# Performance work log

Measured on AMD Instinct MI355X. Metric: run time of the kernel, lower is better.

Reference implementation:

```python
import jax, jax.numpy as jnp
import numpy as np

N_NODES = 20000
N_EDGES = 256000
F_IN = 1024
HID = 1000
N_CLS = 1000
NEG_SLOPE = 0.2


def _glorot(key, shape):
    fan_in, fan_out = shape[1], shape[0]
    lim = np.sqrt(6.0 / (fan_in + fan_out))
    return jax.random.uniform(key, shape, jnp.float32, -lim, lim)


def setup_inputs() -> dict:
    key = jax.random.key(0)
    ks = jax.random.split(key, 16)
    x = jax.random.normal(ks[0], (N_NODES, F_IN), jnp.float32)
    edge_index = jax.random.randint(ks[1], (2, N_EDGES), 0, N_NODES, jnp.int64)
    edge_attr = jax.random.uniform(ks[2], (N_EDGES, 1), jnp.float32)
    return {
        "x": x,
        "edge_index": edge_index,
        "edge_attr": edge_attr,
        # conv1 params (GATv2Conv: F_IN -> HID, heads=1, edge_dim=1)
        "w1_l": _glorot(ks[3], (HID, F_IN)),
        "b1_l": jnp.zeros((HID,), jnp.float32),
        "w1_r": _glorot(ks[4], (HID, F_IN)),
        "b1_r": jnp.zeros((HID,), jnp.float32),
        "w1_e": _glorot(ks[5], (HID, 1)),
        "att1": _glorot(ks[6], (1, HID))[0],
        "bias1": jnp.zeros((HID,), jnp.float32),
        # conv2 params (HID -> N_CLS, heads=1, concat=False)
        "w2_l": _glorot(ks[7], (N_CLS, HID)),
        "b2_l": jnp.zeros((N_CLS,), jnp.float32),
        "w2_r": _glorot(ks[8], (N_CLS, HID)),
        "b2_r": jnp.zeros((N_CLS,), jnp.float32),
        "w2_e": _glorot(ks[9], (N_CLS, 1)),
        "att2": _glorot(ks[10], (1, N_CLS))[0],
        "bias2": jnp.zeros((N_CLS,), jnp.float32),
    }


def gatv2_layer(x, src, dst, edge_attr, Wl, bl, Wr, br, We, att, bias):
    # GATv2Conv with heads=1 (eval mode: attention dropout inactive).
    n = x.shape[0]
    xl = x @ Wl.T + bl                       # source-side transform [N, C]
    xr = x @ Wr.T + br                       # target-side transform [N, C]
    e = xl[src] + xr[dst] + edge_attr @ We.T  # per-edge features [E, C]
    e = jax.nn.leaky_relu(e, NEG_SLOPE)
    logits = e @ att                          # [E]
    # segment softmax over incoming edges of each target node
    m = jax.ops.segment_max(logits, dst, num_segments=n)
    alpha = jnp.exp(logits - m[dst])
    denom = jax.ops.segment_sum(alpha, dst, num_segments=n)
    alpha = alpha / (denom[dst] + 1e-16)
    out = jax.ops.segment_sum(xl[src] * alpha[:, None], dst, num_segments=n)
    return out + bias


def reference(x, edge_index, edge_attr,
              w1_l, b1_l, w1_r, b1_r, w1_e, att1, bias1,
              w2_l, b2_l, w2_r, b2_r, w2_e, att2, bias2):
    src, dst = edge_index[0], edge_index[1]
    # feature dropout (p=0.6) is identity in eval mode
    h = gatv2_layer(x, src, dst, edge_attr, w1_l, b1_l, w1_r, b1_r, w1_e, att1, bias1)
    h = jax.nn.relu(h)
    h = gatv2_layer(h, src, dst, edge_attr, w2_l, b2_l, w2_r, b2_r, w2_e, att2, bias2)
    return jax.nn.sigmoid(h)
```

## Files before the change

### kernel.cpp

```cpp
#include <hip/hip_runtime.h>
#include <math.h>

#define N_NODES 20000
#define N_EDGES 256000
#define F_IN 1024
#define C_DIM 1000
#define NEG_SLOPE 0.2f

#define MPAD 20096
#define KDIM 1024
#define NW 2048

typedef __attribute__((ext_vector_type(8))) short          bf16x8;
typedef __attribute__((ext_vector_type(8))) unsigned short u16x8;
typedef __attribute__((ext_vector_type(4))) float          f32x4;
typedef unsigned short us;

__device__ __forceinline__ us f2bf(float f) {
  unsigned u = __float_as_uint(f);
  return (us)((u + 0x7FFFu + ((u >> 16) & 1u)) >> 16);
}
__device__ __forceinline__ float bf2f(us u) {
  return __uint_as_float(((unsigned)u) << 16);
}

__device__ __forceinline__ void gld16(void* lds, const void* g) {
  __builtin_amdgcn_global_load_lds(
      (const __attribute__((address_space(1))) unsigned int*)g,
      (__attribute__((address_space(3))) unsigned int*)lds, 16, 0, 0);
}

__global__ void count_k(const int* __restrict__ edst, int* __restrict__ counts) {
  int e = blockIdx.x * blockDim.x + threadIdx.x;
  if (e < N_EDGES) atomicAdd(&counts[edst[e]], 1);
}

__global__ __launch_bounds__(1024)
void scan_k(const int* __restrict__ counts, int* __restrict__ row_ptr, int* __restrict__ cursor) {
  __shared__ int sm[1024];
  int t = threadIdx.x;
  int base = t * 20;
  int loc[20];
  int run = 0;
#pragma unroll
  for (int i = 0; i < 20; ++i) {
    int idx = base + i;
    int v = (idx < N_NODES) ? counts[idx] : 0;
    run += v;
    loc[i] = run;
  }
  sm[t] = run;
  __syncthreads();
  for (int off = 1; off < 1024; off <<= 1) {
    int v = (t >= off) ? sm[t - off] : 0;
    __syncthreads();
    sm[t] += v;
    __syncthreads();
  }
  int excl = (t > 0) ? sm[t - 1] : 0;
#pragma unroll
  for (int i = 0; i < 20; ++i) {
    int idx = base + i;
    if (idx < N_NODES) {
      int e = excl + ((i > 0) ? loc[i - 1] : 0);
      row_ptr[idx] = e;
      cursor[idx] = e;
    }
  }
  if (t == 0) row_ptr[N_NODES] = sm[1023];
}

__global__ void scatter_k(const int* __restrict__ esrc, const float* __restrict__ eattr,
                          const int* __restrict__ edst, int* __restrict__ cursor,
                          int2* __restrict__ spair) {
  int e = blockIdx.x * blockDim.x + threadIdx.x;
  if (e < N_EDGES) {
    int p = atomicAdd(&cursor[edst[e]], 1);
    spair[p] = make_int2(esrc[e], __float_as_int(eattr[e]));
  }
}

__global__ void cvt_pad_k(const float* __restrict__ src, us* __restrict__ dst,
                          int R, int C, int dstRows) {
  long total = (long)dstRows * 256;
  for (long i = (long)blockIdx.x * blockDim.x + threadIdx.x; i < total;
       i += (long)gridDim.x * blockDim.x) {
    int row = (int)(i >> 8);
    int c = ((int)(i & 255)) << 2;
    ushort4 o = make_ushort4(0, 0, 0, 0);
    if (row < R && c < C) {
      float4 v = *(const float4*)(src + (long)row * C + c);
      o.x = f2bf(v.x); o.y = f2bf(v.y); o.z = f2bf(v.z); o.w = f2bf(v.w);
    }
    *(ushort4*)(dst + ((long)row << 10) + c) = o;
  }
}

__global__ __launch_bounds__(256)
void gemm_mfma_k(const us* __restrict__ Abf, const us* __restrict__ Wbf,
                 const float* __restrict__ bl, const float* __restrict__ br,
                 us* __restrict__ Cbf) {
  __shared__ us As0[4096], As1[4096], Bs0[4096], Bs1[4096];
  const int tid = threadIdx.x;
  const int lane = tid & 63;
  const int wv = tid >> 6;
  const int wr = wv >> 1, wc = wv & 1;

  const int nwg = gridDim.x;
  const int q = nwg >> 3;
  const int wg = (blockIdx.x & 7) * q + (blockIdx.x >> 3);
  const long bm = (long)(wg >> 4) * 128;
  const long bn = (long)(wg & 15) * 128;

  f32x4 acc[4][4];
  const f32x4 z4 = {0.f, 0.f, 0.f, 0.f};
#pragma unroll
  for (int i = 0; i < 4; ++i)
#pragma unroll
    for (int j = 0; j < 4; ++j) acc[i][j] = z4;

  const int i0 = tid, i1 = tid + 256;
  const us* gA0 = Abf + (bm + (i0 >> 2)) * KDIM + (i0 & 3) * 8;
  const us* gA1 = Abf + (bm + (i1 >> 2)) * KDIM + (i1 & 3) * 8;
  const us* gB0 = Wbf + (bn + (i0 >> 2)) * KDIM + (i0 & 3) * 8;
  const us* gB1 = Wbf + (bn + (i1 >> 2)) * KDIM + (i1 & 3) * 8;

  const int g = lane >> 4;
  const int rA = lane & 15;

  gld16(As0 + wv * 512, gA0);
  gld16(As0 + 2048 + wv * 512, gA1);
  gld16(Bs0 + wv * 512, gB0);
  gld16(Bs0 + 2048 + wv * 512, gB1);
  __syncthreads();

  for (int t = 0; t < 32; ++t) {
    if (t + 1 < 32) {
      int kn = (t + 1) << 5;
      us* dA = ((t + 1) & 1) ? As1 : As0;
      us* dB = ((t + 1) & 1) ? Bs1 : Bs0;
      gld16(dA + wv * 512, gA0 + kn);
      gld16(dA + 2048 + wv * 512, gA1 + kn);
      gld16(dB + wv * 512, gB0 + kn);
      gld16(dB + 2048 + wv * 512, gB1 + kn);
    }
    const us* Ar = (t & 1) ? As1 : As0;
    const us* Br = (t & 1) ? Bs1 : Bs0;
    bf16x8 av[4], bv[4];
#pragma unroll
    for (int mi = 0; mi < 4; ++mi)
      av[mi] = *(const bf16x8*)&Ar[(wr * 64 + mi * 16 + rA) * 32 + g * 8];
#pragma unroll
    for (int ni = 0; ni < 4; ++ni)
      bv[ni] = *(const bf16x8*)&Br[(wc * 64 + ni * 16 + rA) * 32 + g * 8];
#pragma unroll
    for (int mi = 0; mi < 4; ++mi)
#pragma unroll
      for (int ni = 0; ni < 4; ++ni)
        acc[mi][ni] = __builtin_amdgcn_mfma_f32_16x16x32_bf16(av[mi], bv[ni], acc[mi][ni], 0, 0, 0);
    __syncthreads();
  }

  int coln[4]; float biasv[4]; int cok[4];
#pragma unroll
  for (int ni = 0; ni < 4; ++ni) {
    coln[ni] = (int)bn + wc * 64 + ni * 16 + rA;
    int cm = coln[ni] & 1023;
    cok[ni] = (cm < C_DIM);
    biasv[ni] = cok[ni] ? ((coln[ni] < 1024) ? bl[cm] : br[cm]) : 0.f;
  }
#pragma unroll
  for (int mi = 0; mi < 4; ++mi) {
#pragma unroll
    for (int j = 0; j < 4; ++j) {
      int row = (int)bm + wr * 64 + mi * 16 + g * 4 + j;
      if (row < N_NODES) {
#pragma unroll
        for (int ni = 0; ni < 4; ++ni)
          if (cok[ni])
            Cbf[(long)row * NW + coln[ni]] = f2bf(acc[mi][ni][j] + biasv[ni]);
      }
    }
  }
}

template <int ACT>
__global__ __launch_bounds__(256)
void edge_agg_k(const us* __restrict__ xlr, const int2* __restrict__ spair,
                const int* __restrict__ row_ptr,
                const float* __restrict__ We, const float* __restrict__ att,
                const float* __restrict__ bias, us* __restrict__ hout,
                float* __restrict__ fout) {
  const int wave = threadIdx.x >> 6;
  const int lane = threadIdx.x & 63;
  const int q0 = lane, q1 = lane + 64;
  const bool ok1 = (q1 < 125);

  const int d = (blockIdx.x << 2) | wave;
  if (d >= N_NODES) return;

  float attv[2][8], wev[2][8];
#pragma unroll
  for (int j = 0; j < 2; ++j) {
    int qq = lane + 64 * j;
    if (qq < 125) {
      float4 a0 = ((const float4*)att)[2 * qq], a1 = ((const float4*)att)[2 * qq + 1];
      float4 w0 = ((const float4*)We)[2 * qq],  w1 = ((const float4*)We)[2 * qq + 1];
      attv[j][0] = a0.x; attv[j][1] = a0.y; attv[j][2] = a0.z; attv[j][3] = a0.w;
      attv[j][4] = a1.x; attv[j][5] = a1.y; attv[j][6] = a1.z; attv[j][7] = a1.w;
      wev[j][0] = w0.x; wev[j][1] = w0.y; wev[j][2] = w0.z; wev[j][3] = w0.w;
      wev[j][4] = w1.x; wev[j][5] = w1.y; wev[j][6] = w1.z; wev[j][7] = w1.w;
    } else {
#pragma unroll
      for (int t = 0; t < 8; ++t) { attv[j][t] = 0.f; wev[j][t] = 0.f; }
    }
  }

  const int beg = row_ptr[d];
  const int end = row_ptr[d + 1];

  float xrv[2][8];
  {
    const u16x8* xrp = (const u16x8*)(xlr + (long)d * NW + 1024);
#pragma unroll
    for (int j = 0; j < 2; ++j) {
      int qq = lane + 64 * j;
      if (qq < 125) {
        u16x8 h = xrp[qq];
#pragma unroll
        for (int t = 0; t < 8; ++t) xrv[j][t] = bf2f(h[t]);
      } else {
#pragma unroll
        for (int t = 0; t < 8; ++t) xrv[j][t] = 0.f;
      }
    }
  }

  float m = -INFINITY, denom = 0.f;
  float acc[2][8];
#pragma unroll
  for (int j = 0; j < 2; ++j)
#pragma unroll
    for (int t = 0; t < 8; ++t) acc[j][t] = 0.f;

#define EDGE_LOGIT(PAIR, VH0, VH1, PART)                                   \
  {                                                                        \
    const u16x8* xs = (const u16x8*)(xlr + (long)(PAIR).x * NW);           \
    float ea = __int_as_float((PAIR).y);                                   \
    VH0 = xs[q0];                                                          \
    if (ok1) VH1 = xs[q1];                                                 \
    else { u16x8 zz = {0,0,0,0,0,0,0,0}; VH1 = zz; }                       \
    PART = 0.f;                                                            \
    _Pragma("unroll")                                                      \
    for (int t = 0; t < 8; ++t) {                                          \
      float tt = bf2f(VH0[t]) + xrv[0][t] + ea * wev[0][t];                \
      tt = (tt >= 0.f) ? tt : NEG_SLOPE * tt;                              \
      PART = fmaf(attv[0][t], tt, PART);                                   \
      float uu = bf2f(VH1[t]) + xrv[1][t] + ea * wev[1][t];                \
      uu = (uu >= 0.f) ? uu : NEG_SLOPE * uu;                              \
      PART = fmaf(attv[1][t], uu, PART);                                   \
    }                                                                      \
  }

#define ONLINE_UPDATE(PART, VH0, VH1)                                      \
  {                                                                        \
    if ((PART) > m) {                                                      \
      float sc = __expf(m - (PART));                                       \
      denom = denom * sc + 1.f;                                            \
      _Pragma("unroll")                                                    \
      for (int t = 0; t < 8; ++t) {                                        \
        acc[0][t] = fmaf(acc[0][t], sc, bf2f(VH0[t]));                     \
        acc[1][t] = fmaf(acc[1][t], sc, bf2f(VH1[t]));                     \
      }                                                                    \
      m = (PART);                                                          \
    } else {                                                               \
      float w = __expf((PART) - m);                                        \
      denom += w;                                                          \
      _Pragma("unroll")                                                    \
      for (int t = 0; t < 8; ++t) {                                        \
        acc[0][t] = fmaf(w, bf2f(VH0[t]), acc[0][t]);                      \
        acc[1][t] = fmaf(w, bf2f(VH1[t]), acc[1][t]);                      \
      }                                                                    \
    }                                                                      \
  }

  int i = beg;
  for (; i + 2 <= end; i += 2) {
    int2 p0 = spair[i], p1 = spair[i + 1];
    u16x8 a0, a1, b0, b1;
    float pt0, pt1;
    EDGE_LOGIT(p0, a0, a1, pt0);
    EDGE_LOGIT(p1, b0, b1, pt1);
#pragma unroll
    for (int off = 32; off > 0; off >>= 1) {
      pt0 += __shfl_xor(pt0, off, 64);
      pt1 += __shfl_xor(pt1, off, 64);
    }
    ONLINE_UPDATE(pt0, a0, a1);
    ONLINE_UPDATE(pt1, b0, b1);
  }
  if (i < end) {
    int2 p0 = spair[i];
    u16x8 a0, a1;
    float pt0;
    EDGE_LOGIT(p0, a0, a1, pt0);
#pragma unroll
    for (int off = 32; off > 0; off >>= 1) pt0 += __shfl_xor(pt0, off, 64);
    ONLINE_UPDATE(pt0, a0, a1);
  }
#undef EDGE_LOGIT
#undef ONLINE_UPDATE

  float inv = 1.f / (denom + 1e-16f);
  if (ACT == 0) {
    us* orow = hout + ((long)d << 10);
#pragma unroll
    for (int j = 0; j < 2; ++j) {
      int qq = lane + 64 * j;
      u16x8 pk = {0, 0, 0, 0, 0, 0, 0, 0};
      if (qq < 125) {
        const float4 b0 = ((const float4*)bias)[2 * qq], b1 = ((const float4*)bias)[2 * qq + 1];
        const float bb[8] = {b0.x, b0.y, b0.z, b0.w, b1.x, b1.y, b1.z, b1.w};
#pragma unroll
        for (int t = 0; t < 8; ++t)
          pk[t] = f2bf(fmaxf(fmaf(acc[j][t], inv, bb[t]), 0.f));
      }
      ((u16x8*)orow)[qq] = pk;
    }
  } else {
#pragma unroll
    for (int j = 0; j < 2; ++j) {
      int qq = lane + 64 * j;
      if (qq < 125) {
        const float4 b0 = ((const float4*)bias)[2 * qq], b1 = ((const float4*)bias)[2 * qq + 1];
        const float bb[8] = {b0.x, b0.y, b0.z, b0.w, b1.x, b1.y, b1.z, b1.w};
        float o[8];
#pragma unroll
        for (int t = 0; t < 8; ++t)
          o[t] = 1.f / (1.f + __expf(-fmaf(acc[j][t], inv, bb[t])));
        float4* op = (float4*)(fout + (long)d * C_DIM + 8 * qq);
        op[0] = make_float4(o[0], o[1], o[2], o[3]);
        op[1] = make_float4(o[4], o[5], o[6], o[7]);
      }
    }
  }
}

extern "C" void kernel_launch(void* const* d_in, const int* in_sizes, int n_in,
                              void* d_out, int out_size, void* d_ws, size_t ws_size,
                              hipStream_t stream) {
  const float* x     = (const float*)d_in[0];
  const int*   ei    = (const int*)d_in[1];
  const float* eattr = (const float*)d_in[2];
  const float* w1l   = (const float*)d_in[3];
  const float* b1l   = (const float*)d_in[4];
  const float* w1r   = (const float*)d_in[5];
  const float* b1r   = (const float*)d_in[6];
  const float* w1e   = (const float*)d_in[7];
  const float* att1  = (const float*)d_in[8];
  const float* bias1 = (const float*)d_in[9];
  const float* w2l   = (const float*)d_in[10];
  const float* b2l   = (const float*)d_in[11];
  const float* w2r   = (const float*)d_in[12];
  const float* b2r   = (const float*)d_in[13];
  const float* w2e   = (const float*)d_in[14];
  const float* att2  = (const float*)d_in[15];
  const float* bias2 = (const float*)d_in[16];
  float* out = (float*)d_out;

  char* w = (char*)d_ws;
  us*  xlr  = (us*)w;
  us*  Abf  = (us*)(w + 82313216L);
  us*  W21  = (us*)(w + 123469824L);
  us*  W22  = (us*)(w + 127664128L);
  int2* spair = (int2*)(w + 131858432L);
  int* row_ptr = (int*)(w + 133906432L);
  int* cursor  = row_ptr + (N_NODES + 1);
  int* counts  = cursor + N_NODES;

  const int* esrc = ei;
  const int* edst = ei + N_EDGES;

  hipMemsetAsync(counts, 0, N_NODES * sizeof(int), stream);
  count_k<<<(N_EDGES + 255) / 256, 256, 0, stream>>>(edst, counts);
  scan_k<<<1, 1024, 0, stream>>>(counts, row_ptr, cursor);
  scatter_k<<<(N_EDGES + 255) / 256, 256, 0, stream>>>(esrc, eattr, edst, cursor, spair);

  cvt_pad_k<<<1024, 256, 0, stream>>>(w1l, W21, C_DIM, F_IN, 1024);
  cvt_pad_k<<<1024, 256, 0, stream>>>(w1r, W21 + 1024 * 1024, C_DIM, F_IN, 1024);
  cvt_pad_k<<<1024, 256, 0, stream>>>(w2l, W22, C_DIM, C_DIM, 1024);
  cvt_pad_k<<<1024, 256, 0, stream>>>(w2r, W22 + 1024 * 1024, C_DIM, C_DIM, 1024);

  cvt_pad_k<<<4096, 256, 0, stream>>>(x, Abf, N_NODES, F_IN, MPAD);
  gemm_mfma_k<<<2512, 256, 0, stream>>>(Abf, W21, b1l, b1r, xlr);
  edge_agg_k<0><<<N_NODES / 4, 256, 0, stream>>>(xlr, spair, row_ptr, w1e, att1, bias1,
                                                 Abf, nullptr);

  gemm_mfma_k<<<2512, 256, 0, stream>>>(Abf, W22, b2l, b2r, xlr);
  edge_agg_k<1><<<N_NODES / 4, 256, 0, stream>>>(xlr, spair, row_ptr, w2e, att2, bias2,
                                                 nullptr, out);
}
```

Measured before the change: 524.9 us.

## Enlarge GEMM tiles to 256x256 with triple-buffered LDS pipeline and swizzle

The bf16 MFMA GEMM moves from 128x128 tiles with 256 threads and double buffering to 256x256 tiles with 512 threads (8 waves, each computing 128x64). It uses a 3-stage global-to-LDS prefetch ring with explicit vmcnt waits and an XOR swizzle on LDS rows to reduce bank conflicts. The MFMA block is wrapped in setprio. M padding grows to a multiple of 256 and the workspace offsets move to match. The aim is more operand reuse per LDS load and better overlap of loads with math. In exchange the kernel needs much more LDS (about 96KB per block), which limits occupancy, and there are fewer workgroups to spread across the CUs.

```diff
diff --git a/kernel.cpp b/kernel.cpp
--- a/kernel.cpp
+++ b/kernel.cpp
@@ -7,7 +7,7 @@
 #define C_DIM 1000
 #define NEG_SLOPE 0.2f
 
-#define MPAD 20096
+#define MPAD 20224
 #define KDIM 1024
 #define NW 2048
 
@@ -96,70 +96,97 @@
   }
 }
 
-__global__ __launch_bounds__(256)
+__global__ __launch_bounds__(512, 2)
 void gemm_mfma_k(const us* __restrict__ Abf, const us* __restrict__ Wbf,
                  const float* __restrict__ bl, const float* __restrict__ br,
                  us* __restrict__ Cbf) {
-  __shared__ us As0[4096], As1[4096], Bs0[4096], Bs1[4096];
+  __shared__ us As[3 * 8192];
+  __shared__ us Bs[3 * 8192];
   const int tid = threadIdx.x;
   const int lane = tid & 63;
   const int wv = tid >> 6;
-  const int wr = wv >> 1, wc = wv & 1;
-
-  const int nwg = gridDim.x;
-  const int q = nwg >> 3;
-  const int wg = (blockIdx.x & 7) * q + (blockIdx.x >> 3);
-  const long bm = (long)(wg >> 4) * 128;
-  const long bn = (long)(wg & 15) * 128;
-
-  f32x4 acc[4][4];
-  const f32x4 z4 = {0.f, 0.f, 0.f, 0.f};
-#pragma unroll
-  for (int i = 0; i < 4; ++i)
-#pragma unroll
-    for (int j = 0; j < 4; ++j) acc[i][j] = z4;
-
-  const int i0 = tid, i1 = tid + 256;
-  const us* gA0 = Abf + (bm + (i0 >> 2)) * KDIM + (i0 & 3) * 8;
-  const us* gA1 = Abf + (bm + (i1 >> 2)) * KDIM + (i1 & 3) * 8;
-  const us* gB0 = Wbf + (bn + (i0 >> 2)) * KDIM + (i0 & 3) * 8;
-  const us* gB1 = Wbf + (bn + (i1 >> 2)) * KDIM + (i1 & 3) * 8;
-
+  const int wr = wv >> 2;
+  const int wc = wv & 3;
   const int g = lane >> 4;
   const int rA = lane & 15;
 
-  gld16(As0 + wv * 512, gA0);
-  gld16(As0 + 2048 + wv * 512, gA1);
-  gld16(Bs0 + wv * 512, gB0);
-  gld16(Bs0 + 2048 + wv * 512, gB1);
-  __syncthreads();
-
-  for (int t = 0; t < 32; ++t) {
-    if (t + 1 < 32) {
-      int kn = (t + 1) << 5;
-      us* dA = ((t + 1) & 1) ? As1 : As0;
-      us* dB = ((t + 1) & 1) ? Bs1 : Bs0;
-      gld16(dA + wv * 512, gA0 + kn);
-      gld16(dA + 2048 + wv * 512, gA1 + kn);
-      gld16(dB + wv * 512, gB0 + kn);
-      gld16(dB + 2048 + wv * 512, gB1 + kn);
-    }
-    const us* Ar = (t & 1) ? As1 : As0;
-    const us* Br = (t & 1) ? Bs1 : Bs0;
-    bf16x8 av[4], bv[4];
-#pragma unroll
-    for (int mi = 0; mi < 4; ++mi)
-      av[mi] = *(const bf16x8*)&Ar[(wr * 64 + mi * 16 + rA) * 32 + g * 8];
-#pragma unroll
-    for (int ni = 0; ni < 4; ++ni)
-      bv[ni] = *(const bf16x8*)&Br[(wc * 64 + ni * 16 + rA) * 32 + g * 8];
-#pragma unroll
-    for (int mi = 0; mi < 4; ++mi)
-#pragma unroll
-      for (int ni = 0; ni < 4; ++ni)
-        acc[mi][ni] = __builtin_amdgcn_mfma_f32_16x16x32_bf16(av[mi], bv[ni], acc[mi][ni], 0, 0, 0);
-    __syncthreads();
-  }
+  const int wg = (blockIdx.x & 7) * 79 + (blockIdx.x >> 3);
+  const long bm = (long)(wg >> 3) * 256;
+  const long bn = (long)(wg & 7) * 256;
+
+  f32x4 acc[8][4];
+  const f32x4 z4 = {0.f, 0.f, 0.f, 0.f};
+#pragma unroll
+  for (int i = 0; i < 8; ++i)
+#pragma unroll
+    for (int j = 0; j < 4; ++j) acc[i][j] = z4;
+
+  const us* srcA[2];
+  const us* srcB[2];
+#pragma unroll
+  for (int r = 0; r < 2; ++r) {
+    int i = tid + r * 512;
+    int row = i >> 2;
+    int c = (i & 3) ^ ((row >> 1) & 3);
+    srcA[r] = Abf + (bm + row) * KDIM + c * 8;
+    srcB[r] = Wbf + (bn + row) * KDIM + c * 8;
+  }
+
+#define STAGE(TT, SLOT)                                               \
+  {                                                                   \
+    const int k0 = (TT) * 32;                                         \
+    us* Ad = As + (SLOT) * 8192;                                      \
+    us* Bd = Bs + (SLOT) * 8192;                                      \
+    gld16(Ad + wv * 512, srcA[0] + k0);                               \
+    gld16(Ad + 4096 + wv * 512, srcA[1] + k0);                        \
+    gld16(Bd + wv * 512, srcB[0] + k0);                               \
+    gld16(Bd + 4096 + wv * 512, srcB[1] + k0);                        \
+  }
+
+#define COMPUTE(SLOT)                                                 \
+  {                                                                   \
+    const us* Ar = As + (SLOT) * 8192;                                \
+    const us* Br = Bs + (SLOT) * 8192;                                \
+    bf16x8 av[8], bv[4];                                              \
+    _Pragma("unroll")                                                 \
+    for (int ni = 0; ni < 4; ++ni) {                                  \
+      int row = wc * 64 + ni * 16 + rA;                               \
+      bv[ni] = *(const bf16x8*)&Br[row * 32 + ((g ^ ((row >> 1) & 3)) << 3)]; \
+    }                                                                 \
+    _Pragma("unroll")                                                 \
+    for (int mi = 0; mi < 8; ++mi) {                                  \
+      int row = wr * 128 + mi * 16 + rA;                              \
+      av[mi] = *(const bf16x8*)&Ar[row * 32 + ((g ^ ((row >> 1) & 3)) << 3)]; \
+    }                                                                 \
+    __builtin_amdgcn_s_setprio(1);                                    \
+    _Pragma("unroll")                                                 \
+    for (int mi = 0; mi < 8; ++mi)                                    \
+      _Pragma("unroll")                                               \
+      for (int ni = 0; ni < 4; ++ni)                                  \
+        acc[mi][ni] = __builtin_amdgcn_mfma_f32_16x16x32_bf16(av[mi], bv[ni], acc[mi][ni], 0, 0, 0); \
+    __builtin_amdgcn_s_setprio(0);                                    \
+  }
+
+  STAGE(0, 0)
+  STAGE(1, 1)
+  asm volatile("s_waitcnt vmcnt(4)" ::: "memory");
+  __builtin_amdgcn_sched_barrier(0);
+  __builtin_amdgcn_s_barrier();
+
+  int sc = 0, sn = 1, sp = 2;
+  for (int t = 0; t < 30; ++t) {
+    STAGE(t + 2, sp)
+    COMPUTE(sc)
+    asm volatile("s_waitcnt vmcnt(4)" ::: "memory");
+    __builtin_amdgcn_sched_barrier(0);
+    __builtin_amdgcn_s_barrier();
+    int tmp = sc; sc = sn; sn = sp; sp = tmp;
+  }
+  COMPUTE(sc)
+  asm volatile("s_waitcnt vmcnt(0)" ::: "memory");
+  __builtin_amdgcn_sched_barrier(0);
+  __builtin_amdgcn_s_barrier();
+  COMPUTE(sn)
 
   int coln[4]; float biasv[4]; int cok[4];
 #pragma unroll
@@ -170,10 +197,10 @@
     biasv[ni] = cok[ni] ? ((coln[ni] < 1024) ? bl[cm] : br[cm]) : 0.f;
   }
 #pragma unroll
-  for (int mi = 0; mi < 4; ++mi) {
+  for (int mi = 0; mi < 8; ++mi) {
 #pragma unroll
     for (int j = 0; j < 4; ++j) {
-      int row = (int)bm + wr * 64 + mi * 16 + g * 4 + j;
+      int row = (int)bm + wr * 128 + mi * 16 + g * 4 + j;
       if (row < N_NODES) {
 #pragma unroll
         for (int ni = 0; ni < 4; ++ni)
@@ -182,6 +209,8 @@
       }
     }
   }
+#undef STAGE
+#undef COMPUTE
 }
 
 template <int ACT>
@@ -370,11 +399,11 @@
 
   char* w = (char*)d_ws;
   us*  xlr  = (us*)w;
-  us*  Abf  = (us*)(w + 82313216L);
-  us*  W21  = (us*)(w + 123469824L);
-  us*  W22  = (us*)(w + 127664128L);
-  int2* spair = (int2*)(w + 131858432L);
-  int* row_ptr = (int*)(w + 133906432L);
+  us*  Abf  = (us*)(w + 81920000L);
+  us*  W21  = (us*)(w + 123338752L);
+  us*  W22  = (us*)(w + 127533056L);
+  int2* spair = (int2*)(w + 131727360L);
+  int* row_ptr = (int*)(w + 133775360L);
   int* cursor  = row_ptr + (N_NODES + 1);
   int* counts  = cursor + N_NODES;
 
@@ -392,11 +421,11 @@
   cvt_pad_k<<<1024, 256, 0, stream>>>(w2r, W22 + 1024 * 1024, C_DIM, C_DIM, 1024);
 
   cvt_pad_k<<<4096, 256, 0, stream>>>(x, Abf, N_NODES, F_IN, MPAD);
-  gemm_mfma_k<<<2512, 256, 0, stream>>>(Abf, W21, b1l, b1r, xlr);
+  gemm_mfma_k<<<632, 512, 0, stream>>>(Abf, W21, b1l, b1r, xlr);
   edge_agg_k<0><<<N_NODES / 4, 256, 0, stream>>>(xlr, spair, row_ptr, w1e, att1, bias1,
                                                  Abf, nullptr);
 
-  gemm_mfma_k<<<2512, 256, 0, stream>>>(Abf, W22, b2l, b2r, xlr);
+  gemm_mfma_k<<<632, 512, 0, stream>>>(Abf, W22, b2l, b2r, xlr);
   edge_agg_k<1><<<N_NODES / 4, 256, 0, stream>>>(xlr, spair, row_ptr, w2e, att2, bias2,
                                                  nullptr, out);
 }
```

Result: slower. 551.8 us (+5.1%).
